# Performance work log

Measured on AMD Instinct MI355X. Metric: run time of the kernel, lower is better.

## Reference

```python
import jax, jax.numpy as jnp
import numpy as np

C_T, C_Z, C_HID, N_HEADS = 64, 128, 16, 4
N_TEMPL, N_RES = 4, 512
INF = 1e9


def setup_inputs() -> dict:
    key = jax.random.key(0)
    ks = jax.random.split(key, 7)
    return {
        "t": jax.random.normal(ks[0], (N_TEMPL, N_RES, N_RES, C_T), jnp.float32),
        "z": jax.random.normal(ks[1], (N_RES, N_RES, C_Z), jnp.float32),
        "template_mask": jnp.ones((N_TEMPL,), jnp.float32),
        "wq": jax.random.normal(ks[2], (C_Z, N_HEADS * C_HID), jnp.float32) * 0.05,
        "wk": jax.random.normal(ks[3], (C_T, N_HEADS * C_HID), jnp.float32) * 0.05,
        "wv": jax.random.normal(ks[4], (C_T, N_HEADS * C_HID), jnp.float32) * 0.05,
        "wo": jax.random.normal(ks[5], (N_HEADS * C_HID, C_Z), jnp.float32) * 0.05,
        "bo": jnp.zeros((C_Z,), jnp.float32),
    }


def reference(t, z, template_mask, wq, wk, wv, wo, bo):
    # t: [S, N, N, C_t]  z: [N, N, C_z]  template_mask: [S]
    h, d = N_HEADS, C_HID
    bias = INF * (template_mask - 1.0)  # [S], 0 for kept, -inf for masked
    tp = jnp.transpose(t, (1, 2, 0, 3))  # [N, N, S, C_t] (permute_final_dims (1,2,0,3))
    scale = 1.0 / jnp.sqrt(jnp.asarray(d, z.dtype))
    q = jnp.einsum("ijc,chd->ijhd", z, wq.reshape(C_Z, h, d)) * scale  # [N,N,h,d]
    k = jnp.einsum("ijsc,chd->ijshd", tp, wk.reshape(C_T, h, d))       # [N,N,S,h,d]
    v = jnp.einsum("ijsc,chd->ijshd", tp, wv.reshape(C_T, h, d))
    logits = jnp.einsum("ijhd,ijshd->ijhs", q, k) + bias  # [N,N,h,S]
    a = jax.nn.softmax(logits, axis=-1)
    o = jnp.einsum("ijhs,ijshd->ijhd", a, v).reshape(N_RES, N_RES, h * d)
    out = o @ wo + bo  # [N, N, C_z]
    out = out * (jnp.sum(template_mask) > 0).astype(out.dtype)
    return out
```

## Files before the change

kernel.cpp:

```cpp
#include <hip/hip_runtime.h>

#define NRES 512
#define CZ   128
#define CT   64

typedef short bf16x8 __attribute__((ext_vector_type(8)));
typedef float f32x4  __attribute__((ext_vector_type(4)));

#define MFMA16(a,b,c) __builtin_amdgcn_mfma_f32_16x16x32_bf16((a),(b),(c),0,0,0)

__device__ __forceinline__ unsigned short f2bf(float f){
  unsigned int u = __builtin_bit_cast(unsigned int, f);
  u += 0x7fffu + ((u >> 16) & 1u);
  return (unsigned short)(u >> 16);
}
__device__ __forceinline__ float bf2f(short b){
  return __builtin_bit_cast(float, ((unsigned int)(unsigned short)b) << 16);
}
__device__ __forceinline__ bf16x8 pack8(const float4 a, const float4 b){
  bf16x8 r;
  r[0]=(short)f2bf(a.x); r[1]=(short)f2bf(a.y); r[2]=(short)f2bf(a.z); r[3]=(short)f2bf(a.w);
  r[4]=(short)f2bf(b.x); r[5]=(short)f2bf(b.y); r[6]=(short)f2bf(b.z); r[7]=(short)f2bf(b.w);
  return r;
}

__global__ void prep_pack(const float* __restrict__ wq, const float* __restrict__ wk,
                          const float* __restrict__ wv, const float* __restrict__ wo,
                          unsigned short* __restrict__ packed){
  int idx = blockIdx.x * 256 + threadIdx.x;
  if (idx >= 48 * 64) return;
  int f = idx >> 6, lane = idx & 63;
  const float* W; int Ncols, nt, ks; float scale = 1.0f;
  if (f < 16)      { W = wq; Ncols = 64;  nt = f >> 2;        ks = f & 3;        scale = 0.25f; }
  else if (f < 24) { W = wk; Ncols = 64;  nt = (f - 16) >> 1; ks = (f - 16) & 1; }
  else if (f < 32) { W = wv; Ncols = 64;  nt = (f - 24) >> 1; ks = (f - 24) & 1; }
  else             { W = wo; Ncols = 128; nt = (f - 32) >> 1; ks = (f - 32) & 1; }
  int col = nt * 16 + (lane & 15);
  int k0  = ks * 32 + (lane >> 4) * 8;
  unsigned short* dst = packed + (size_t)f * 512 + (size_t)lane * 8;
#pragma unroll
  for (int j = 0; j < 8; ++j)
    dst[j] = f2bf(W[(k0 + j) * Ncols + col] * scale);
}

__launch_bounds__(256, 3)
__global__ void tpa_main(const float* __restrict__ t, const float* __restrict__ z,
                         const float* __restrict__ mask, const float* __restrict__ bo,
                         const unsigned short* __restrict__ packed,
                         float* __restrict__ out){
  __shared__ __align__(16) char smem[37888];

  const int tid  = threadIdx.x;
  const int lane = tid & 63;
  const int w    = tid >> 6;
  const int cl   = lane & 15;
  const int g    = lane >> 4;
  const int b    = blockIdx.x;
  const int i    = b >> 3;
  const int j0   = (b & 7) << 6;
  const int r0   = j0 + (w << 4);
  const int grow = r0 + cl;

  const float4* zp = reinterpret_cast<const float4*>(z + ((size_t)i * NRES + grow) * CZ);
  float4 zr[8];
#pragma unroll
  for (int ks = 0; ks < 4; ++ks)
#pragma unroll
    for (int p = 0; p < 2; ++p)
      zr[ks * 2 + p] = zp[ks * 8 + g * 2 + p];

#pragma unroll
  for (int s = 0; s < 4; ++s){
    const float4* tp4 = reinterpret_cast<const float4*>(
        t + (((size_t)s * NRES + i) * NRES + r0) * CT);
    char* tb = smem + (w * 4 + s) * 2048;
#pragma unroll
    for (int it = 0; it < 4; ++it){
      int idx = it * 64 + lane;
      float4 v = tp4[idx];
      int row = idx >> 4, c4 = idx & 15;
      unsigned int lo = (unsigned int)f2bf(v.x) | ((unsigned int)f2bf(v.y) << 16);
      unsigned int hi = (unsigned int)f2bf(v.z) | ((unsigned int)f2bf(v.w) << 16);
      *reinterpret_cast<uint2*>(tb + row * 128 + ((c4 * 8) ^ ((row & 7) << 4))) =
          make_uint2(lo, hi);
    }
  }

  bf16x8 za[4];
#pragma unroll
  for (int ks = 0; ks < 4; ++ks) za[ks] = pack8(zr[ks * 2], zr[ks * 2 + 1]);

  float m0 = mask[0], m1 = mask[1], m2 = mask[2], m3 = mask[3];
  float msum = m0 + m1 + m2 + m3;
  float bias[4] = {1e9f * (m0 - 1.0f), 1e9f * (m1 - 1.0f),
                   1e9f * (m2 - 1.0f), 1e9f * (m3 - 1.0f)};

  bf16x8 ta[4][2];
#pragma unroll
  for (int s = 0; s < 4; ++s){
    const char* tb = smem + (w * 4 + s) * 2048;
#pragma unroll
    for (int ks = 0; ks < 2; ++ks)
      ta[s][ks] = *reinterpret_cast<const bf16x8*>(
          tb + cl * 128 + ((ks * 64 + g * 16) ^ ((cl & 7) << 4)));
  }

#define LOADB(fi) (*reinterpret_cast<const bf16x8*>(packed + (size_t)(fi) * 512 + (size_t)lane * 8))

  float* a_ws = reinterpret_cast<float*>(smem + 32768 + w * 1280);

#pragma unroll
  for (int h = 0; h < 4; ++h){
    f32x4 q = {0.f, 0.f, 0.f, 0.f};
#pragma unroll
    for (int ks = 0; ks < 4; ++ks) q = MFMA16(za[ks], LOADB(h * 4 + ks), q);

    f32x4 lgh[4];
#pragma unroll
    for (int s = 0; s < 4; ++s){
      f32x4 acc = {0.f, 0.f, 0.f, 0.f};
      acc = MFMA16(ta[s][0], LOADB(16 + h * 2 + 0), acc);
      acc = MFMA16(ta[s][1], LOADB(16 + h * 2 + 1), acc);
      f32x4 p = acc * q;
#pragma unroll
      for (int off = 1; off < 16; off <<= 1){
#pragma unroll
        for (int r = 0; r < 4; ++r) p[r] += __shfl_xor(p[r], off);
      }
#pragma unroll
      for (int r = 0; r < 4; ++r) p[r] += bias[s];
      lgh[s] = p;
    }
    f32x4 mx, sum = {0.f, 0.f, 0.f, 0.f};
#pragma unroll
    for (int r = 0; r < 4; ++r)
      mx[r] = fmaxf(fmaxf(lgh[0][r], lgh[1][r]), fmaxf(lgh[2][r], lgh[3][r]));
#pragma unroll
    for (int s = 0; s < 4; ++s){
#pragma unroll
      for (int r = 0; r < 4; ++r) lgh[s][r] = __expf(lgh[s][r] - mx[r]);
      sum += lgh[s];
    }
    f32x4 inv;
#pragma unroll
    for (int r = 0; r < 4; ++r) inv[r] = 1.0f / sum[r];
#pragma unroll
    for (int s = 0; s < 4; ++s){
      lgh[s] *= inv;
      if (cl == s * 4 + h)
        *reinterpret_cast<f32x4*>(a_ws + (s * 4 + h) * 20 + (g << 2)) = lgh[s];
    }
  }
  asm volatile("s_waitcnt lgkmcnt(0)" ::: "memory");

  unsigned short* o_ws = reinterpret_cast<unsigned short*>(smem + w * 8192);
#pragma unroll
  for (int h = 0; h < 4; ++h){
    float a0 = a_ws[(0  + h) * 20 + cl];
    float a1 = a_ws[(4  + h) * 20 + cl];
    float a2 = a_ws[(8  + h) * 20 + cl];
    float a3 = a_ws[(12 + h) * 20 + cl];
    bf16x8 ua[2];
#pragma unroll
    for (int ks = 0; ks < 2; ++ks){
#pragma unroll
      for (int j = 0; j < 8; ++j){
        float uu = a0 * bf2f(ta[0][ks][j]) + a1 * bf2f(ta[1][ks][j])
                 + a2 * bf2f(ta[2][ks][j]) + a3 * bf2f(ta[3][ks][j]);
        ua[ks][j] = (short)f2bf(uu);
      }
    }
    f32x4 acc = {0.f, 0.f, 0.f, 0.f};
    acc = MFMA16(ua[0], LOADB(24 + h * 2 + 0), acc);
    acc = MFMA16(ua[1], LOADB(24 + h * 2 + 1), acc);
#pragma unroll
    for (int r = 0; r < 4; ++r){
      int row = (g << 2) + r;
      o_ws[row * 64 + ((h * 16 + cl) ^ ((row & 7) << 3))] = (unsigned short)f2bf(acc[r]);
    }
  }
  asm volatile("s_waitcnt lgkmcnt(0)" ::: "memory");

  {
    bf16x8 oa[2];
#pragma unroll
    for (int ks = 0; ks < 2; ++ks)
      oa[ks] = *reinterpret_cast<const bf16x8*>(
          o_ws + cl * 64 + ((ks * 32 + g * 8) ^ ((cl & 7) << 3)));

    float gate = (msum > 0.0f) ? 1.0f : 0.0f;
    float* outg = out + ((size_t)i * NRES + r0) * CZ;
#pragma unroll
    for (int nt = 0; nt < 8; ++nt){
      f32x4 acc = {0.f, 0.f, 0.f, 0.f};
      acc = MFMA16(oa[0], LOADB(32 + nt * 2 + 0), acc);
      acc = MFMA16(oa[1], LOADB(32 + nt * 2 + 1), acc);
      int col = nt * 16 + cl;
      float bov = bo[col];
#pragma unroll
      for (int r = 0; r < 4; ++r)
        outg[(size_t)((g << 2) + r) * CZ + col] = (acc[r] + bov) * gate;
    }
  }
}

extern "C" void kernel_launch(void* const* d_in, const int* in_sizes, int n_in,
                              void* d_out, int out_size, void* d_ws, size_t ws_size,
                              hipStream_t stream) {
  const float* t    = (const float*)d_in[0];
  const float* z    = (const float*)d_in[1];
  const float* mask = (const float*)d_in[2];
  const float* wq   = (const float*)d_in[3];
  const float* wk   = (const float*)d_in[4];
  const float* wv   = (const float*)d_in[5];
  const float* wo   = (const float*)d_in[6];
  const float* bo   = (const float*)d_in[7];
  unsigned short* packed = (unsigned short*)d_ws;

  hipLaunchKernelGGL(prep_pack, dim3(12), dim3(256), 0, stream, wq, wk, wv, wo, packed);
  hipLaunchKernelGGL(tpa_main, dim3(4096), dim3(256), 0, stream,
                     t, z, mask, bo, packed, (float*)d_out);
}
```

Baseline: 128.0 us.

## Compute V per template via MFMA, DPP reductions, and drop attention LDS staging

Instead of forming the attention-weighted mix of t rows on scalar ALUs and projecting once per head, the kernel now projects V for each template with MFMA and combines it with the softmax weights held in registers. This removes the LDS round trip for attention weights and the scalar bf16 unpack/FMA/repack loop, at the cost of four times as many V-projection MFMAs. The cross-lane sum inside the logit dot product uses DPP row operations instead of shuffle-xor. LDS shrinks to 32 KB and launch bounds are raised to 4 blocks per CU, which tightens the register budget and risks spills.

```diff
diff --git a/kernel.cpp b/kernel.cpp
--- a/kernel.cpp
+++ b/kernel.cpp
@@ -13,15 +13,30 @@
   unsigned int u = __builtin_bit_cast(unsigned int, f);
   u += 0x7fffu + ((u >> 16) & 1u);
   return (unsigned short)(u >> 16);
-}
-__device__ __forceinline__ float bf2f(short b){
-  return __builtin_bit_cast(float, ((unsigned int)(unsigned short)b) << 16);
 }
 __device__ __forceinline__ bf16x8 pack8(const float4 a, const float4 b){
   bf16x8 r;
   r[0]=(short)f2bf(a.x); r[1]=(short)f2bf(a.y); r[2]=(short)f2bf(a.z); r[3]=(short)f2bf(a.w);
   r[4]=(short)f2bf(b.x); r[5]=(short)f2bf(b.y); r[6]=(short)f2bf(b.z); r[7]=(short)f2bf(b.w);
   return r;
+}
+
+template<int CTRL>
+__device__ __forceinline__ float dppadd(float x){
+  int y = __builtin_amdgcn_update_dpp(0, __builtin_bit_cast(int, x), CTRL, 0xF, 0xF, false);
+  return x + __builtin_bit_cast(float, y);
+}
+__device__ __forceinline__ f32x4 reduce16(f32x4 p){
+#pragma unroll
+  for (int r = 0; r < 4; ++r){
+    float v = p[r];
+    v = dppadd<0xB1>(v);
+    v = dppadd<0x4E>(v);
+    v = dppadd<0x141>(v);
+    v = dppadd<0x140>(v);
+    p[r] = v;
+  }
+  return p;
 }
 
 __global__ void prep_pack(const float* __restrict__ wq, const float* __restrict__ wk,
@@ -43,12 +58,12 @@
     dst[j] = f2bf(W[(k0 + j) * Ncols + col] * scale);
 }
 
-__launch_bounds__(256, 3)
+__launch_bounds__(256, 4)
 __global__ void tpa_main(const float* __restrict__ t, const float* __restrict__ z,
                          const float* __restrict__ mask, const float* __restrict__ bo,
                          const unsigned short* __restrict__ packed,
                          float* __restrict__ out){
-  __shared__ __align__(16) char smem[37888];
+  __shared__ __align__(16) char smem[32768];
 
   const int tid  = threadIdx.x;
   const int lane = tid & 63;
@@ -73,7 +88,7 @@
   for (int s = 0; s < 4; ++s){
     const float4* tp4 = reinterpret_cast<const float4*>(
         t + (((size_t)s * NRES + i) * NRES + r0) * CT);
-    char* tb = smem + (w * 4 + s) * 2048;
+    char* tb = smem + w * 8192 + s * 2048;
 #pragma unroll
     for (int it = 0; it < 4; ++it){
       int idx = it * 64 + lane;
@@ -98,7 +113,7 @@
   bf16x8 ta[4][2];
 #pragma unroll
   for (int s = 0; s < 4; ++s){
-    const char* tb = smem + (w * 4 + s) * 2048;
+    const char* tb = smem + w * 8192 + s * 2048;
 #pragma unroll
     for (int ks = 0; ks < 2; ++ks)
       ta[s][ks] = *reinterpret_cast<const bf16x8*>(
@@ -107,7 +122,7 @@
 
 #define LOADB(fi) (*reinterpret_cast<const bf16x8*>(packed + (size_t)(fi) * 512 + (size_t)lane * 8))
 
-  float* a_ws = reinterpret_cast<float*>(smem + 32768 + w * 1280);
+  unsigned short* o_ws = reinterpret_cast<unsigned short*>(smem + w * 8192);
 
 #pragma unroll
   for (int h = 0; h < 4; ++h){
@@ -121,12 +136,7 @@
       f32x4 acc = {0.f, 0.f, 0.f, 0.f};
       acc = MFMA16(ta[s][0], LOADB(16 + h * 2 + 0), acc);
       acc = MFMA16(ta[s][1], LOADB(16 + h * 2 + 1), acc);
-      f32x4 p = acc * q;
-#pragma unroll
-      for (int off = 1; off < 16; off <<= 1){
-#pragma unroll
-        for (int r = 0; r < 4; ++r) p[r] += __shfl_xor(p[r], off);
-      }
+      f32x4 p = reduce16(acc * q);
 #pragma unroll
       for (int r = 0; r < 4; ++r) p[r] += bias[s];
       lgh[s] = p;
@@ -145,38 +155,20 @@
 #pragma unroll
     for (int r = 0; r < 4; ++r) inv[r] = 1.0f / sum[r];
 #pragma unroll
+    for (int s = 0; s < 4; ++s) lgh[s] *= inv;
+
+    f32x4 of = {0.f, 0.f, 0.f, 0.f};
+#pragma unroll
     for (int s = 0; s < 4; ++s){
-      lgh[s] *= inv;
-      if (cl == s * 4 + h)
-        *reinterpret_cast<f32x4*>(a_ws + (s * 4 + h) * 20 + (g << 2)) = lgh[s];
-    }
-  }
-  asm volatile("s_waitcnt lgkmcnt(0)" ::: "memory");
-
-  unsigned short* o_ws = reinterpret_cast<unsigned short*>(smem + w * 8192);
-#pragma unroll
-  for (int h = 0; h < 4; ++h){
-    float a0 = a_ws[(0  + h) * 20 + cl];
-    float a1 = a_ws[(4  + h) * 20 + cl];
-    float a2 = a_ws[(8  + h) * 20 + cl];
-    float a3 = a_ws[(12 + h) * 20 + cl];
-    bf16x8 ua[2];
-#pragma unroll
-    for (int ks = 0; ks < 2; ++ks){
-#pragma unroll
-      for (int j = 0; j < 8; ++j){
-        float uu = a0 * bf2f(ta[0][ks][j]) + a1 * bf2f(ta[1][ks][j])
-                 + a2 * bf2f(ta[2][ks][j]) + a3 * bf2f(ta[3][ks][j]);
-        ua[ks][j] = (short)f2bf(uu);
-      }
-    }
-    f32x4 acc = {0.f, 0.f, 0.f, 0.f};
-    acc = MFMA16(ua[0], LOADB(24 + h * 2 + 0), acc);
-    acc = MFMA16(ua[1], LOADB(24 + h * 2 + 1), acc);
+      f32x4 vacc = {0.f, 0.f, 0.f, 0.f};
+      vacc = MFMA16(ta[s][0], LOADB(24 + h * 2 + 0), vacc);
+      vacc = MFMA16(ta[s][1], LOADB(24 + h * 2 + 1), vacc);
+      of += lgh[s] * vacc;
+    }
 #pragma unroll
     for (int r = 0; r < 4; ++r){
       int row = (g << 2) + r;
-      o_ws[row * 64 + ((h * 16 + cl) ^ ((row & 7) << 3))] = (unsigned short)f2bf(acc[r]);
+      o_ws[row * 64 + ((h * 16 + cl) ^ ((row & 7) << 3))] = (unsigned short)f2bf(of[r]);
     }
   }
   asm volatile("s_waitcnt lgkmcnt(0)" ::: "memory");
```

New measurement: 157.0 us. 1.23x slower.
